# Kernel tuning notes

Hardware: AMD Instinct MI355X
Metric: run time of the kernel (lower is better)

## Reference

```python
import jax, jax.numpy as jnp
import numpy as np

EMB = 1024
H = 16
DH = 64


def setup_inputs() -> dict:
    key = jax.random.key(0)
    ks = jax.random.split(key, 9)
    s = 1.0 / np.sqrt(EMB)
    so = 1.0 / np.sqrt(H * DH)
    return {
        "x": jax.random.normal(ks[0], (4, 2048, EMB), dtype=jnp.float32),
        "Wq": jax.random.uniform(ks[1], (H * DH, EMB), jnp.float32, -s, s),
        "bq": jax.random.uniform(ks[2], (H * DH,), jnp.float32, -s, s),
        "Wk": jax.random.uniform(ks[3], (H * DH, EMB), jnp.float32, -s, s),
        "bk": jax.random.uniform(ks[4], (H * DH,), jnp.float32, -s, s),
        "Wv": jax.random.uniform(ks[5], (H * DH, EMB), jnp.float32, -s, s),
        "bv": jax.random.uniform(ks[6], (H * DH,), jnp.float32, -s, s),
        "Wo": jax.random.uniform(ks[7], (EMB, H * DH), jnp.float32, -so, so),
        "bo": jax.random.uniform(ks[8], (EMB,), jnp.float32, -so, so),
    }


def reference(x, Wq, bq, Wk, bk, Wv, bv, Wo, bo):
    B, S, E = x.shape
    # project and split heads: [B, H, S, Dh]
    def proj(W, b):
        return (jnp.einsum('bse,de->bsd', x, W) + b).reshape(B, S, H, DH).transpose(0, 2, 1, 3)
    q = proj(Wq, bq)
    k = proj(Wk, bk)
    v = proj(Wv, bv)
    scores = jnp.einsum('bhsd,bhtd->bhst', q / jnp.sqrt(jnp.float32(DH)), k)
    attn = jax.nn.softmax(scores, axis=-1)
    out = jnp.einsum('bhst,bhtd->bhsd', attn, v)  # [B,H,S,Dh]
    out = out.transpose(0, 2, 1, 3).reshape(B, S, H * DH)
    return jnp.einsum('bsd,ed->bse', out, Wo) + bo
```

## Files before the change

kernel.cpp:

```cpp
#include <hip/hip_runtime.h>
#include <hip/hip_bf16.h>
#include <stdint.h>

typedef __bf16 bf16x8 __attribute__((ext_vector_type(8)));
typedef float f32x4 __attribute__((ext_vector_type(4)));
typedef float f32x16 __attribute__((ext_vector_type(16)));
typedef uint32_t u32x4 __attribute__((ext_vector_type(4)));

__device__ __forceinline__ ushort f2bf(float f) {
  uint32_t u = __builtin_bit_cast(uint32_t, f);
  u += 0x7FFFu + ((u >> 16) & 1u);
  return (ushort)(u >> 16);
}

__device__ __forceinline__ uint32_t cvtpk(float lo, float hi) {
  uint32_t r;
  asm("v_cvt_pk_bf16_f32 %0, %1, %2" : "=v"(r) : "v"(lo), "v"(hi));
  return r;
}

__device__ __forceinline__ void p32swap(uint32_t& x, uint32_t& y) {
  asm("v_permlane32_swap_b32 %0, %1" : "+v"(x), "+v"(y));
}

__device__ __forceinline__ void gload16(const void* g, void* l) {
  auto gp = reinterpret_cast<const __attribute__((address_space(1))) char*>(
      reinterpret_cast<uintptr_t>(g));
  auto lp = reinterpret_cast<__attribute__((address_space(3))) char*>(
      reinterpret_cast<uintptr_t>(l));
  __builtin_amdgcn_global_load_lds(gp, lp, 16, 0, 0);
}

__device__ __forceinline__ f32x4 mfma16(bf16x8 a, bf16x8 b, f32x4 c) {
  return __builtin_amdgcn_mfma_f32_16x16x32_bf16(a, b, c, 0, 0, 0);
}
__device__ __forceinline__ f32x16 mfma32(bf16x8 a, bf16x8 b, f32x16 c) {
  return __builtin_amdgcn_mfma_f32_32x32x16_bf16(a, b, c, 0, 0, 0);
}

#define LGKM0 do { asm volatile("s_waitcnt lgkmcnt(0)" ::: "memory"); \
                   __builtin_amdgcn_sched_barrier(0); } while (0)
#define VMW(n) do { asm volatile("s_waitcnt vmcnt(" #n ")" ::: "memory"); \
                    __builtin_amdgcn_sched_barrier(0); } while (0)
#define SBAR __builtin_amdgcn_s_barrier()

__global__ void cast_kernel(const float* __restrict__ src, ushort* __restrict__ dst) {
  int i = (blockIdx.x * 256 + threadIdx.x) * 4;
  float4 v = *(const float4*)(src + i);
  ushort4 o;
  o.x = f2bf(v.x); o.y = f2bf(v.y); o.z = f2bf(v.z); o.w = f2bf(v.w);
  *(ushort4*)(dst + i) = o;
}

template <int MODE>
__global__ __launch_bounds__(512, 2) void gemm_k(
    const ushort* __restrict__ A, const ushort* __restrict__ W,
    const float* __restrict__ b0, const float* __restrict__ b1,
    const float* __restrict__ b2,
    ushort* __restrict__ qo, ushort* __restrict__ ko, ushort* __restrict__ vo,
    float* __restrict__ fo)
{
  __shared__ ushort As[2][128 * 64];
  __shared__ ushort Bs[2][256 * 64];
  const int tid = threadIdx.x;
  const int lane = tid & 63, wid = tid >> 6;
  const int wr = wid >> 2, wc = wid & 3;
  const int l15 = lane & 15, l4 = lane >> 4;

  const int wg = blockIdx.x, nwg = gridDim.x, qch = nwg >> 3;
  const int lid = (wg & 7) * qch + (wg >> 3);
  const int bx = lid >> 6, by = lid & 63;
  const int m0 = by * 128, n0 = bx * 256;

  const char* Ag = (const char*)(A + (size_t)m0 * 1024);
  const char* Wg = (const char*)(W + (size_t)n0 * 1024);

  f32x4 acc[4][4] = {};

  const int soff = tid * 16;
  const int srowA0 = soff >> 7, scolb = soff & 127;

  auto STAGE = [&](int d, int kt) {
    const int k0b = kt * 128;
#pragma unroll
    for (int s = 0; s < 2; ++s) {
      int off = soff + s * 8192;
      int row = off >> 7, cb = off & 127;
      int sc = cb ^ ((row & 7) << 4);
      gload16(Ag + (size_t)row * 2048 + k0b + sc, (char*)As[d] + off);
    }
#pragma unroll
    for (int s = 0; s < 4; ++s) {
      int off = soff + s * 8192;
      int row = off >> 7, cb = off & 127;
      int sc = cb ^ ((row & 7) << 4);
      gload16(Wg + (size_t)row * 2048 + k0b + sc, (char*)Bs[d] + off);
    }
  };

  bf16x8 af[4][2], bfr[4][2];

  auto EXTRACT = [&](int d) {
#pragma unroll
    for (int mt = 0; mt < 4; ++mt) {
      int row = wr * 64 + mt * 16 + l15;
      int sw = (row & 7) << 4;
#pragma unroll
      for (int kk = 0; kk < 2; ++kk)
        af[mt][kk] = *(const bf16x8*)((const char*)As[d] + row * 128 +
                                      ((kk * 64 + l4 * 16) ^ sw));
    }
#pragma unroll
    for (int nt = 0; nt < 4; ++nt) {
      int row = wc * 64 + nt * 16 + l15;
      int sw = (row & 7) << 4;
#pragma unroll
      for (int kk = 0; kk < 2; ++kk)
        bfr[nt][kk] = *(const bf16x8*)((const char*)Bs[d] + row * 128 +
                                       ((kk * 64 + l4 * 16) ^ sw));
    }
  };

  auto MFMAS = [&]() {
    __builtin_amdgcn_s_setprio(1);
#pragma unroll
    for (int kk = 0; kk < 2; ++kk)
#pragma unroll
      for (int mt = 0; mt < 4; ++mt)
#pragma unroll
        for (int nt = 0; nt < 4; ++nt)
          acc[mt][nt] = mfma16(af[mt][kk], bfr[nt][kk], acc[mt][nt]);
    __builtin_amdgcn_s_setprio(0);
  };

  STAGE(0, 0);
  STAGE(1, 1);
  VMW(6); SBAR;

#pragma unroll 2
  for (int t = 0; t < 14; ++t) {
    const int d = t & 1;
    EXTRACT(d);
    LGKM0;
    SBAR;
    STAGE(d, t + 2);
    MFMAS();
    VMW(6); SBAR;
  }
  EXTRACT(0); LGKM0; SBAR; MFMAS(); VMW(0); SBAR;
  EXTRACT(1); LGKM0; MFMAS();

  if (MODE == 0) {
    const int seg = n0 >> 10;
    const int nb = n0 & 1023;
    const float* bptr = (seg == 0) ? b0 : (seg == 1) ? b1 : b2;
#pragma unroll
    for (int nt = 0; nt < 4; ++nt) {
      int nl = nb + wc * 64 + nt * 16 + l15;
      int h = nl >> 6, dd = nl & 63;
      float bias = bptr[nl];
#pragma unroll
      for (int mt = 0; mt < 4; ++mt) {
        int m = m0 + wr * 64 + mt * 16 + l4 * 4;
        int b = m >> 11, s = m & 2047;
        if (seg == 2) {
          ushort4 pk;
          pk.x = f2bf(acc[mt][nt][0] + bias);
          pk.y = f2bf(acc[mt][nt][1] + bias);
          pk.z = f2bf(acc[mt][nt][2] + bias);
          pk.w = f2bf(acc[mt][nt][3] + bias);
          *(ushort4*)(vo + (size_t)((b * 16 + h) * 64 + dd) * 2048 + s) = pk;
        } else {
          ushort* dst = (seg == 0) ? qo : ko;
          float sc = (seg == 0) ? 0.18033688011112042f : 1.0f;
#pragma unroll
          for (int r = 0; r < 4; ++r)
            dst[(size_t)((b * 16 + h) * 2048 + s + r) * 64 + dd] =
                f2bf((acc[mt][nt][r] + bias) * sc);
        }
      }
    }
  } else {
#pragma unroll
    for (int nt = 0; nt < 4; ++nt) {
      int n = n0 + wc * 64 + nt * 16 + l15;
      float bias = b0[n];
#pragma unroll
      for (int mt = 0; mt < 4; ++mt) {
        int m = m0 + wr * 64 + mt * 16 + l4 * 4;
#pragma unroll
        for (int r = 0; r < 4; ++r)
          fo[(size_t)(m + r) * 1024 + n] = acc[mt][nt][r] + bias;
      }
    }
  }
}

__global__ __launch_bounds__(256, 4) void attn_k(
    const ushort* __restrict__ Q, const ushort* __restrict__ K,
    const ushort* __restrict__ V, ushort* __restrict__ O)
{
  __shared__ ushort KVs[2][8192];
  const int tid = threadIdx.x, lane = tid & 63;
  const int l31 = lane & 31, hi = lane >> 5;
  const int w = tid >> 6;
  const int bh = blockIdx.x;
  const int b = bh >> 4, h = bh & 15;
  const int q = blockIdx.y * 128 + w * 32 + l31;
  const ushort* Qh = Q + (size_t)bh * 131072;
  const ushort* Kh = K + (size_t)bh * 131072;
  const ushort* Vh = V + (size_t)bh * 131072;

  bf16x8 qf[4];
#pragma unroll
  for (int c = 0; c < 4; ++c)
    qf[c] = *(const bf16x8*)(Qh + (size_t)q * 64 + c * 16 + hi * 8);

  u32x4 onebits;
  onebits[0] = 0x3F803F80u; onebits[1] = 0x3F803F80u;
  onebits[2] = 0x3F803F80u; onebits[3] = 0x3F803F80u;
  const bf16x8 ones = __builtin_bit_cast(bf16x8, onebits);

  f32x16 oacc[2] = {};
  float mrun = -INFINITY, lrun = 0.f;

  const int sw = (l31 & 7) << 4;
  const int loff = tid * 16;
  const int srow = loff >> 7, scolb = loff & 127;

  auto STAGE = [&](int buf, int j) {
    char* base = (char*)KVs[buf];
#pragma unroll
    for (int sh = 0; sh < 2; ++sh) {
      int row = srow + sh * 32;
      int off = loff + sh * 4096;
      int sc = scolb ^ ((row & 7) << 4);
      gload16((const char*)Kh + (size_t)j * 8192 + row * 128 + sc, base + off);
      gload16((const char*)Vh + (size_t)row * 4096 + j * 128 + sc, base + 8192 + off);
    }
  };

  STAGE(0, 0);
  __syncthreads();
  int cur = 0;

  for (int j = 0; j < 32; ++j) {
    if (j < 31) STAGE(cur ^ 1, j + 1);
    const char* Kb = (const char*)KVs[cur];
    const char* Vb = Kb + 8192;

    f32x16 sacc[2] = {};
    __builtin_amdgcn_s_setprio(1);
#pragma unroll
    for (int t = 0; t < 2; ++t)
#pragma unroll
      for (int c = 0; c < 4; ++c) {
        bf16x8 kfr = *(const bf16x8*)(Kb + (t * 32 + l31) * 128 +
                                      ((c * 32 + hi * 16) ^ sw));
        sacc[t] = mfma32(kfr, qf[c], sacc[t]);
      }
    __builtin_amdgcn_s_setprio(0);

    float a0 = fmaxf(sacc[0][0], sacc[0][1]);
    float a1 = fmaxf(sacc[0][8], sacc[0][9]);
    float a2 = fmaxf(sacc[1][0], sacc[1][1]);
    float a3 = fmaxf(sacc[1][8], sacc[1][9]);
#pragma unroll
    for (int r = 2; r < 8; ++r) {
      a0 = fmaxf(a0, fmaxf(sacc[0][r], sacc[0][r + 8]));
      a2 = fmaxf(a2, fmaxf(sacc[1][r], sacc[1][r + 8]));
    }
    a1 = fmaxf(a1, a3);
    float pm = fmaxf(fmaxf(a0, a2), a1);
    pm = fmaxf(pm, __shfl_xor(pm, 32));

    if (!__all(pm - mrun <= 8.0f)) {
      float mnew = fmaxf(mrun, pm);
      float f = __builtin_amdgcn_exp2f(mrun - mnew);
      lrun *= f;
#pragma unroll
      for (int dt = 0; dt < 2; ++dt)
#pragma unroll
        for (int r = 0; r < 16; ++r) oacc[dt][r] *= f;
      mrun = mnew;
    }

#pragma unroll
    for (int t = 0; t < 2; ++t)
#pragma unroll
      for (int r = 0; r < 16; ++r)
        sacc[t][r] = __builtin_amdgcn_exp2f(sacc[t][r] - mrun);

    uint32_t wlo[2][4], whi[2][4];
#pragma unroll
    for (int t = 0; t < 2; ++t)
#pragma unroll
      for (int g = 0; g < 4; ++g) {
        wlo[t][g] = cvtpk(sacc[t][g * 4 + 0], sacc[t][g * 4 + 1]);
        whi[t][g] = cvtpk(sacc[t][g * 4 + 2], sacc[t][g * 4 + 3]);
      }

    bf16x8 pb[4];
#pragma unroll
    for (int c = 0; c < 4; ++c) {
      const int t = c >> 1, gb = (c & 1) * 2;
      uint32_t x0 = wlo[t][gb], y0 = wlo[t][gb + 1];
      p32swap(x0, y0);
      uint32_t x1 = whi[t][gb], y1 = whi[t][gb + 1];
      p32swap(x1, y1);
      u32x4 wv_;
      wv_[0] = x0; wv_[1] = x1; wv_[2] = y0; wv_[3] = y1;
      pb[c] = __builtin_bit_cast(bf16x8, wv_);
    }

    f32x16 ssacc = {};
    __builtin_amdgcn_s_setprio(1);
#pragma unroll
    for (int dt = 0; dt < 2; ++dt)
#pragma unroll
      for (int c = 0; c < 4; ++c) {
        bf16x8 vfr = *(const bf16x8*)(Vb + (dt * 32 + l31) * 128 +
                                      ((c * 32 + hi * 16) ^ sw));
        oacc[dt] = mfma32(vfr, pb[c], oacc[dt]);
      }
#pragma unroll
    for (int c = 0; c < 4; ++c)
      ssacc = mfma32(ones, pb[c], ssacc);
    __builtin_amdgcn_s_setprio(0);
    lrun += ssacc[0];

    __syncthreads();
    cur ^= 1;
  }

  float linv = 1.0f / lrun;
  ushort* Ob = O + (size_t)(b * 2048 + q) * 1024 + h * 64;
#pragma unroll
  for (int dt = 0; dt < 2; ++dt)
#pragma unroll
    for (int g = 0; g < 4; ++g) {
      ushort4 o4;
      o4.x = f2bf(oacc[dt][g * 4 + 0] * linv);
      o4.y = f2bf(oacc[dt][g * 4 + 1] * linv);
      o4.z = f2bf(oacc[dt][g * 4 + 2] * linv);
      o4.w = f2bf(oacc[dt][g * 4 + 3] * linv);
      *(ushort4*)(Ob + dt * 32 + g * 8 + hi * 4) = o4;
    }
}

extern "C" void kernel_launch(void* const* d_in, const int* in_sizes, int n_in,
                              void* d_out, int out_size, void* d_ws, size_t ws_size,
                              hipStream_t stream)
{
  const float* x  = (const float*)d_in[0];
  const float* Wq = (const float*)d_in[1];
  const float* bq = (const float*)d_in[2];
  const float* Wk = (const float*)d_in[3];
  const float* bk = (const float*)d_in[4];
  const float* Wv = (const float*)d_in[5];
  const float* bv = (const float*)d_in[6];
  const float* Wo = (const float*)d_in[7];
  const float* bo = (const float*)d_in[8];
  float* out = (float*)d_out;
  ushort* ws = (ushort*)d_ws;

  ushort* xb   = ws;
  ushort* wqkv = ws + 8388608;
  ushort* wo   = ws + 11534336;
  ushort* qb   = ws + 12582912;
  ushort* kb   = ws + 20971520;
  ushort* vb   = ws + 29360128;

  cast_kernel<<<8192, 256, 0, stream>>>(x, xb);
  cast_kernel<<<1024, 256, 0, stream>>>(Wq, wqkv);
  cast_kernel<<<1024, 256, 0, stream>>>(Wk, wqkv + 1048576);
  cast_kernel<<<1024, 256, 0, stream>>>(Wv, wqkv + 2097152);
  cast_kernel<<<1024, 256, 0, stream>>>(Wo, wo);

  gemm_k<0><<<768, 512, 0, stream>>>(xb, wqkv, bq, bk, bv, qb, kb, vb, nullptr);
  attn_k<<<dim3(64, 16), 256, 0, stream>>>(qb, kb, vb, xb);
  gemm_k<1><<<256, 512, 0, stream>>>(xb, wo, bo, bo, bo, nullptr, nullptr, nullptr, out);
}
```

Measured before the change: 199.0 us.

## Software-pipeline QK^T one tile ahead with triple-buffered K in attention

The attention kernel splits the shared K/V buffer into a triple-buffered K ring and a double-buffered V ring. It computes the QK^T scores for the next key tile during the current iteration's softmax and PV work, ping-ponging two score register sets. The goal is to overlap MFMA score computation with the exp/convert work and hide LDS/global latency. In exchange it uses more registers and lowers the launch-bounds occupancy hint from 4 to 3 blocks per CU.

```diff
diff --git a/kernel.cpp b/kernel.cpp
--- a/kernel.cpp
+++ b/kernel.cpp
@@ -78,7 +78,6 @@
   f32x4 acc[4][4] = {};
 
   const int soff = tid * 16;
-  const int srowA0 = soff >> 7, scolb = soff & 127;
 
   auto STAGE = [&](int d, int kt) {
     const int k0b = kt * 128;
@@ -196,11 +195,12 @@
   }
 }
 
-__global__ __launch_bounds__(256, 4) void attn_k(
+__global__ __launch_bounds__(256, 3) void attn_k(
     const ushort* __restrict__ Q, const ushort* __restrict__ K,
     const ushort* __restrict__ V, ushort* __restrict__ O)
 {
-  __shared__ ushort KVs[2][8192];
+  __shared__ ushort Kbuf[3][4096];
+  __shared__ ushort Vbuf[2][4096];
   const int tid = threadIdx.x, lane = tid & 63;
   const int l31 = lane & 31, hi = lane >> 5;
   const int w = tid >> 6;
@@ -228,28 +228,30 @@
   const int loff = tid * 16;
   const int srow = loff >> 7, scolb = loff & 127;
 
-  auto STAGE = [&](int buf, int j) {
-    char* base = (char*)KVs[buf];
+  auto STAGE_K = [&](int slot, int j) {
+    char* base = (char*)Kbuf[slot];
 #pragma unroll
     for (int sh = 0; sh < 2; ++sh) {
       int row = srow + sh * 32;
       int off = loff + sh * 4096;
       int sc = scolb ^ ((row & 7) << 4);
       gload16((const char*)Kh + (size_t)j * 8192 + row * 128 + sc, base + off);
-      gload16((const char*)Vh + (size_t)row * 4096 + j * 128 + sc, base + 8192 + off);
-    }
-  };
-
-  STAGE(0, 0);
-  __syncthreads();
-  int cur = 0;
-
-  for (int j = 0; j < 32; ++j) {
-    if (j < 31) STAGE(cur ^ 1, j + 1);
-    const char* Kb = (const char*)KVs[cur];
-    const char* Vb = Kb + 8192;
-
-    f32x16 sacc[2] = {};
+    }
+  };
+  auto STAGE_V = [&](int slot, int j) {
+    char* base = (char*)Vbuf[slot];
+#pragma unroll
+    for (int sh = 0; sh < 2; ++sh) {
+      int row = srow + sh * 32;
+      int off = loff + sh * 4096;
+      int sc = scolb ^ ((row & 7) << 4);
+      gload16((const char*)Vh + (size_t)row * 4096 + j * 128 + sc, base + off);
+    }
+  };
+
+  auto QKc = [&](const char* Kb, f32x16 (&out)[2]) {
+    out[0] = f32x16{};
+    out[1] = f32x16{};
     __builtin_amdgcn_s_setprio(1);
 #pragma unroll
     for (int t = 0; t < 2; ++t)
@@ -257,21 +259,34 @@
       for (int c = 0; c < 4; ++c) {
         bf16x8 kfr = *(const bf16x8*)(Kb + (t * 32 + l31) * 128 +
                                       ((c * 32 + hi * 16) ^ sw));
-        sacc[t] = mfma32(kfr, qf[c], sacc[t]);
+        out[t] = mfma32(kfr, qf[c], out[t]);
       }
     __builtin_amdgcn_s_setprio(0);
-
-    float a0 = fmaxf(sacc[0][0], sacc[0][1]);
-    float a1 = fmaxf(sacc[0][8], sacc[0][9]);
-    float a2 = fmaxf(sacc[1][0], sacc[1][1]);
-    float a3 = fmaxf(sacc[1][8], sacc[1][9]);
-#pragma unroll
-    for (int r = 2; r < 8; ++r) {
-      a0 = fmaxf(a0, fmaxf(sacc[0][r], sacc[0][r + 8]));
-      a2 = fmaxf(a2, fmaxf(sacc[1][r], sacc[1][r + 8]));
-    }
-    a1 = fmaxf(a1, a3);
-    float pm = fmaxf(fmaxf(a0, a2), a1);
+  };
+
+  int j = 0;
+  int ks = 2;
+  int kr = 1;
+
+  auto body = [&](f32x16 (&cur)[2], f32x16 (&nxt)[2]) {
+    if (j < 30) { STAGE_K(ks, j + 2); ks = (ks == 2) ? 0 : ks + 1; }
+    if (j < 31) {
+      STAGE_V((j + 1) & 1, j + 1);
+      QKc((const char*)Kbuf[0] + kr * 8192, nxt);
+      kr = (kr == 2) ? 0 : kr + 1;
+    }
+
+    float a0 = fmaxf(cur[0][0], fmaxf(cur[0][1], cur[0][2]));
+    float a1 = fmaxf(cur[0][8], fmaxf(cur[0][9], cur[0][10]));
+    float a2 = fmaxf(cur[1][0], fmaxf(cur[1][1], cur[1][2]));
+    float a3 = fmaxf(cur[1][8], fmaxf(cur[1][9], cur[1][10]));
+#pragma unroll
+    for (int r = 3; r < 8; ++r) {
+      a0 = fmaxf(a0, fmaxf(cur[0][r], cur[0][r + 8]));
+      a2 = fmaxf(a2, fmaxf(cur[1][r], cur[1][r + 8]));
+    }
+    a0 = fmaxf(a0, fmaxf(a1, a3));
+    float pm = fmaxf(a0, a2);
     pm = fmaxf(pm, __shfl_xor(pm, 32));
 
     if (!__all(pm - mrun <= 8.0f)) {
@@ -289,15 +304,15 @@
     for (int t = 0; t < 2; ++t)
 #pragma unroll
       for (int r = 0; r < 16; ++r)
-        sacc[t][r] = __builtin_amdgcn_exp2f(sacc[t][r] - mrun);
+        cur[t][r] = __builtin_amdgcn_exp2f(cur[t][r] - mrun);
 
     uint32_t wlo[2][4], whi[2][4];
 #pragma unroll
     for (int t = 0; t < 2; ++t)
 #pragma unroll
       for (int g = 0; g < 4; ++g) {
-        wlo[t][g] = cvtpk(sacc[t][g * 4 + 0], sacc[t][g * 4 + 1]);
-        whi[t][g] = cvtpk(sacc[t][g * 4 + 2], sacc[t][g * 4 + 3]);
+        wlo[t][g] = cvtpk(cur[t][g * 4 + 0], cur[t][g * 4 + 1]);
+        whi[t][g] = cvtpk(cur[t][g * 4 + 2], cur[t][g * 4 + 3]);
       }
 
     bf16x8 pb[4];
@@ -313,6 +328,7 @@
       pb[c] = __builtin_bit_cast(bf16x8, wv_);
     }
 
+    const char* Vb = (const char*)Vbuf[0] + (j & 1) * 8192;
     f32x16 ssacc = {};
     __builtin_amdgcn_s_setprio(1);
 #pragma unroll
@@ -330,7 +346,21 @@
     lrun += ssacc[0];
 
     __syncthreads();
-    cur ^= 1;
+    ++j;
+  };
+
+  STAGE_K(0, 0);
+  STAGE_V(0, 0);
+  STAGE_K(1, 1);
+  __syncthreads();
+
+  f32x16 sA[2], sB[2];
+  QKc((const char*)Kbuf[0], sA);
+
+#pragma unroll 1
+  for (int jj = 0; jj < 16; ++jj) {
+    body(sA, sB);
+    body(sB, sA);
   }
 
   float linv = 1.0f / lrun;
```

New measurement: 215.5 us. +8.3%, slower.
